# Kernel tuning notes

Hardware: AMD Instinct MI355X
Metric: run time of the kernel (lower is better)

The kernel has to match this reference:

```python
import jax, jax.numpy as jnp
import numpy as np
from jax import lax

B, L, V = 64, 48, 50000
E = 300   # emb_dim == repr_dim
F0 = 300  # fc0_dim
F1 = 300  # fc1_dim
NC = 2    # n_classes
NEG = -1e9


def setup_inputs() -> dict:
    key = jax.random.key(0)
    ks = jax.random.split(key, 16)
    inp = {
        "q1": jax.random.randint(ks[0], (B, L), 0, V, dtype=jnp.int64) if jax.config.read('jax_enable_x64') else jax.random.randint(ks[0], (B, L), 0, V, dtype=jnp.int32),
        "q2": jax.random.randint(ks[1], (B, L), 0, V, dtype=jnp.int32),
        "q1_len": jax.random.randint(ks[2], (B,), 1, L + 1, dtype=jnp.int32),
        "q2_len": jax.random.randint(ks[3], (B,), 1, L + 1, dtype=jnp.int32),
        "emb": jax.random.normal(ks[4], (V, E), jnp.float32) * 0.1,
        "conv_w": jax.random.normal(ks[5], (E, E, 3), jnp.float32) * 0.03,
        "conv_b": jnp.zeros((E,), jnp.float32),
        "fc0_w": jax.random.normal(ks[6], (F0, 2 * E), jnp.float32) * 0.04,
        "fc0_b": jnp.zeros((F0,), jnp.float32),
        "fc1_w": jax.random.normal(ks[7], (F1, 2 * F0), jnp.float32) * 0.04,
        "fc1_b": jnp.zeros((F1,), jnp.float32),
        "fc2_w": jax.random.normal(ks[8], (NC, F1), jnp.float32) * 0.05,
        "fc2_b": jnp.zeros((NC,), jnp.float32),
        "att_w": jax.random.normal(ks[9], (1, E + F0), jnp.float32) * 0.05,
        "att_b": jnp.zeros((1,), jnp.float32),
    }
    return inp


def _encode(q, emb, conv_w, conv_b):
    x = emb[q]                                   # [B, L, E]
    x = jnp.transpose(x, (0, 2, 1))              # [B, E, L] (NCW)
    y = lax.conv_general_dilated(x, conv_w, (1,), [(1, 1)],
                                 dimension_numbers=("NCW", "OIW", "NCW"))
    y = jnp.tanh(y + conv_b[None, :, None])
    return jnp.transpose(y, (0, 2, 1))           # [B, L, E]


def reference(q1, q2, q1_len, q2_len, emb, conv_w, conv_b, fc0_w, fc0_b,
              fc1_w, fc1_b, fc2_w, fc2_b, att_w, att_b):
    r1 = _encode(q1, emb, conv_w, conv_b)        # [B, L, E]
    r2 = _encode(q2, emb, conv_w, conv_b)
    pos = jnp.arange(L)
    m1 = pos[None, :] < q1_len[:, None]          # [B, L] valid-token masks
    m2 = pos[None, :] < q2_len[:, None]

    # pairwise features: |r1_i - r2_j| and r1_i * r2_j  -> fc0 -> tanh
    d = jnp.abs(r1[:, :, None, :] - r2[:, None, :, :])   # [B, L1, L2, E]
    p = r1[:, :, None, :] * r2[:, None, :, :]
    Wd, Wp = fc0_w[:, :E], fc0_w[:, E:]
    joint = jnp.tanh(jnp.einsum("bije,fe->bijf", d, Wd)
                     + jnp.einsum("bije,fe->bijf", p, Wp)
                     + fc0_b)                             # [B, L1, L2, F0]

    # masked max-pooling over the other sequence
    s1 = jnp.where(m2[:, None, :, None], joint, NEG).max(axis=2)  # [B, L1, F0]
    s2 = jnp.where(m1[:, :, None, None], joint, NEG).max(axis=1)  # [B, L2, F0]

    # attention-weighted sums (softmax over valid positions only)
    def pool(r, s, m):
        logits = jnp.einsum("bld,d->bl", jnp.concatenate([r, s], -1), att_w[0]) + att_b[0]
        a = jax.nn.softmax(jnp.where(m, logits, NEG), axis=1)     # [B, L]
        return jnp.einsum("bl,blf->bf", a, s)                     # [B, F0]

    h1 = pool(r1, s1, m1)
    h2 = pool(r2, s2, m2)

    j = jnp.tanh(jnp.concatenate([h1, h2], axis=1) @ fc1_w.T + fc1_b)
    return j @ fc2_w.T + fc2_b                                   # [B, 2]
```

## Files before the change

kernel.cpp:

```cpp
#include <hip/hip_runtime.h>
#include <math.h>

#define B_  64
#define L_  48
#define E_  300
#define F0_ 300
#define NEGP (-1e30f)
#define XROW 320
#define RS  312

typedef __attribute__((ext_vector_type(8))) _Float16 half8;
typedef __attribute__((ext_vector_type(8))) short   short8;
typedef __attribute__((ext_vector_type(4))) float   float4v;


__global__ __launch_bounds__(256) void kp_all(
    const int* __restrict__ q1, const int* __restrict__ q2,
    const float* __restrict__ emb, const float* __restrict__ conv_w,
    const float* __restrict__ fc0w,
    _Float16* __restrict__ Bp2, _Float16* __restrict__ Bc,
    _Float16* __restrict__ X)
{
    int u = blockIdx.x * 256 + threadIdx.x;
    if (u < 24320) {
        int m = u >> 8, rest = u & 255;
        int nt = rest >> 6, lane = rest & 63;
        int f = (m / 19) * 64 + nt * 16 + (lane & 15);
        int kb = (m % 19) * 32 + ((lane >> 4) << 3);
        half8 hv;
#pragma unroll
        for (int j = 0; j < 8; ++j) {
            int k = kb + j;
            float v = 0.f;
            if (f < 300) {
                if (k < 300) v = fc0w[f * 600 + k];
                else if (k >= 304 && k < 604) v = fc0w[f * 600 + k - 4];
            }
            hv[j] = (_Float16)v;
        }
        *reinterpret_cast<half8*>(Bp2 + (long)u * 8) = hv;
    } else if (u < 60800) {
        int v = u - 24320;
        int m = v / 1216, rest = v - m * 1216;
        int ntg = rest >> 6, lane = rest & 63;
        int o = ntg * 16 + (lane & 15);
        int kkb = (m % 10) * 32 + ((lane >> 4) << 3);
        int k = m / 10;
        half8 hv;
#pragma unroll
        for (int j = 0; j < 8; ++j) {
            int kk = kkb + j;
            float val = 0.f;
            if (o < 300 && kk < 300) val = conv_w[(o * 300 + kk) * 3 + k];
            hv[j] = (_Float16)val;
        }
        *reinterpret_cast<half8*>(Bc + (long)v * 8) = hv;
    } else if (u < 306560) {
        int v = u - 60800;
        int g = v / 40;
        int e8 = (v - g * 40) * 8;
        int s = g / 3072;
        int rem = g - s * 3072;
        long row = (long)((s ? q2 : q1)[rem]) * 300;
        half8 hv;
        if (e8 + 7 < 300) {
            float4 a = *reinterpret_cast<const float4*>(emb + row + e8);
            float4 c = *reinterpret_cast<const float4*>(emb + row + e8 + 4);
            hv[0] = (_Float16)a.x; hv[1] = (_Float16)a.y; hv[2] = (_Float16)a.z; hv[3] = (_Float16)a.w;
            hv[4] = (_Float16)c.x; hv[5] = (_Float16)c.y; hv[6] = (_Float16)c.z; hv[7] = (_Float16)c.w;
        } else {
#pragma unroll
            for (int j = 0; j < 8; ++j) {
                int i = e8 + j;
                hv[j] = (_Float16)((i < 300) ? emb[row + i] : 0.f);
            }
        }
        *reinterpret_cast<half8*>(X + (long)g * XROW + e8) = hv;
    }
}

__global__ __launch_bounds__(256, 4) void kc_conv(
    const _Float16* __restrict__ X, const _Float16* __restrict__ Bc,
    const float* __restrict__ conv_b, float* __restrict__ r1, float* __restrict__ r2)
{
    int wid = blockIdx.x * 4 + (threadIdx.x >> 6);
    int lane = threadIdx.x & 63;
    int mt = wid / 10;
    int pr = wid - mt * 10;
    int ntg0 = pr * 2;
    bool two = (ntg0 + 1 < 19);
    int row0 = mt * 16;
    int q = lane >> 4, jcol = lane & 15;
    int grow = row0 + jcol;
    int l = grow % 48;

    auto zero8 = []() { half8 z; for (int e = 0; e < 8; ++e) z[e] = (_Float16)0.f; return z; };
    auto loadA = [&](int m) -> half8 {
        int k = m / 10, kk0 = (m - k * 10) * 32;
        int srcl = l + k - 1;
        if (srcl >= 0 && srcl < 48)
            return *reinterpret_cast<const half8*>(X + (long)(grow + k - 1) * XROW + kk0 + q * 8);
        return zero8();
    };
    auto loadB = [&](int m, int ntg) -> half8 {
        return *reinterpret_cast<const half8*>(Bc + ((long)m * 19 + ntg) * 512 + lane * 8);
    };

    float4v acc0 = (float4v){0.f, 0.f, 0.f, 0.f};
    float4v acc1 = (float4v){0.f, 0.f, 0.f, 0.f};

    half8 a_c  = loadA(0);
    half8 b0_c = loadB(0, ntg0);
    half8 b1_c = two ? loadB(0, ntg0 + 1) : b0_c;

    for (int m = 0; m < 30; ++m) {
        half8 a_n, b0_n, b1_n;
        if (m < 29) {
            a_n  = loadA(m + 1);
            b0_n = loadB(m + 1, ntg0);
            b1_n = two ? loadB(m + 1, ntg0 + 1) : b0_n;
        } else { a_n = a_c; b0_n = b0_c; b1_n = b1_c; }
        acc0 = __builtin_amdgcn_mfma_f32_16x16x32_f16(a_c, b0_c, acc0, 0, 0, 0);
        if (two)
            acc1 = __builtin_amdgcn_mfma_f32_16x16x32_f16(a_c, b1_c, acc1, 0, 0, 0);
        a_c = a_n; b0_c = b0_n; b1_c = b1_n;
    }

#pragma unroll
    for (int t = 0; t < 2; ++t) {
        if (t == 1 && !two) break;
        int n = (ntg0 + t) * 16 + jcol;
        if (n >= 300) continue;
        float bias = conv_b[n];
        const float4v& a = t ? acc1 : acc0;
#pragma unroll
        for (int r = 0; r < 4; ++r) {
            int g = row0 + q * 4 + r;
            int s = g / 3072;
            int rem = g - s * 3072;
            float* rout = s ? r2 : r1;
            rout[(long)rem * 300 + n] = tanhf(a[r] + bias);
        }
    }
}

__global__ __launch_bounds__(256, 3) void k2_joint(
    const float* __restrict__ r1, const float* __restrict__ r2,
    const int* __restrict__ q1_len, const int* __restrict__ q2_len,
    const _Float16* __restrict__ Bp2,
    float* __restrict__ s1p, float* __restrict__ s2p)
{
    int x = blockIdx.x;
    int tile = x / 5, nc = x - tile * 5;
    int it = tile / 3, jt = tile - it * 3;
    int b = blockIdx.y;
    int tid = threadIdx.x;
    int q1l = q1_len[b], q2l = q2_len[b];
    long base1 = ((long)(b * 3 + jt) * 48 + it * 16) * 300;
    long base2 = ((long)(b * 3 + it) * 48 + jt * 16) * 300;
    bool active = (it * 16 < q1l) && (jt * 16 < q2l);
    if (!active) {
        for (int idx = tid; idx < 2048; idx += 256) {
            int side = idx >> 10;
            int rest = idx & 1023;
            int row = rest >> 6;
            int f = nc * 64 + (rest & 63);
            if (f < 300) (side ? s2p + base2 : s1p + base1)[row * 300 + f] = NEGP;
        }
        return;
    }

    __shared__ __align__(16) unsigned char smraw[16 * RS * 2 * 2];
    _Float16* r1h = (_Float16*)smraw;
    _Float16* r2h = r1h + 16 * RS;
    float* red = (float*)smraw;

    {
        const float* r1base = r1 + ((long)(b * 48) + it * 16) * 300;
        const float* r2base = r2 + ((long)(b * 48) + jt * 16) * 300;
        for (int u = tid; u < 1200; u += 256) {
            int row = u / 75;
            int e4 = (u - row * 75) * 4;
            float4 v1 = *reinterpret_cast<const float4*>(r1base + row * 300 + e4);
            float4 v2 = *reinterpret_cast<const float4*>(r2base + row * 300 + e4);
            _Float16* d1 = r1h + row * RS + e4;
            _Float16* d2 = r2h + row * RS + e4;
            d1[0] = (_Float16)v1.x; d1[1] = (_Float16)v1.y; d1[2] = (_Float16)v1.z; d1[3] = (_Float16)v1.w;
            d2[0] = (_Float16)v2.x; d2[1] = (_Float16)v2.y; d2[2] = (_Float16)v2.z; d2[3] = (_Float16)v2.w;
        }
        for (int u = tid; u < 2 * 16 * (RS - 300); u += 256) {
            int half = u / (16 * (RS - 300));
            int rest = u - half * 16 * (RS - 300);
            int row = rest / (RS - 300);
            int e = 300 + rest - row * (RS - 300);
            (half ? r2h : r1h)[row * RS + e] = (_Float16)0.f;
        }
    }
    __syncthreads();

    int w    = tid >> 6;
    int lane = tid & 63;
    int q    = lane >> 4;
    int jcol = lane & 15;

    float4v acc[4][4];
#pragma unroll
    for (int mt = 0; mt < 4; ++mt)
#pragma unroll
        for (int nt = 0; nt < 4; ++nt) acc[mt][nt] = (float4v){0.f, 0.f, 0.f, 0.f};

    const _Float16* bbase = Bp2 + (long)(nc * 19) * 2048;
    half8 b0 = *reinterpret_cast<const half8*>(bbase + lane * 8);
    half8 b1 = *reinterpret_cast<const half8*>(bbase + 512 + lane * 8);
    half8 b2 = *reinterpret_cast<const half8*>(bbase + 1024 + lane * 8);
    half8 b3 = *reinterpret_cast<const half8*>(bbase + 1536 + lane * 8);

    for (int kc = 0; kc < 19; ++kc) {
        half8 n0, n1, n2, n3;
        if (kc < 18) {
            const _Float16* nb = bbase + (long)(kc + 1) * 2048;
            n0 = *reinterpret_cast<const half8*>(nb + lane * 8);
            n1 = *reinterpret_cast<const half8*>(nb + 512 + lane * 8);
            n2 = *reinterpret_cast<const half8*>(nb + 1024 + lane * 8);
            n3 = *reinterpret_cast<const half8*>(nb + 1536 + lane * 8);
        } else { n0 = b0; n1 = b1; n2 = b2; n3 = b3; }

        int k0q = kc * 32 + q * 8;
        int koff = (k0q < 304) ? k0q : (k0q - 304);
        const half8 rv2 = *reinterpret_cast<const half8*>(r2h + jcol * RS + koff);
        half8 afr[4];
#pragma unroll
        for (int mt = 0; mt < 4; ++mt) {
            const half8 rv1 = *reinterpret_cast<const half8*>(r1h + (w * 4 + mt) * RS + koff);
            if (k0q < 304) {
                half8 dsub = rv1 - rv2;
                short8 s;
                __builtin_memcpy(&s, &dsub, 16);
                s &= (short)0x7FFF;
                __builtin_memcpy(&afr[mt], &s, 16);
            } else {
                afr[mt] = rv1 * rv2;
            }
        }
#pragma unroll
        for (int mt = 0; mt < 4; ++mt) {
            acc[mt][0] = __builtin_amdgcn_mfma_f32_16x16x32_f16(afr[mt], b0, acc[mt][0], 0, 0, 0);
            acc[mt][1] = __builtin_amdgcn_mfma_f32_16x16x32_f16(afr[mt], b1, acc[mt][1], 0, 0, 0);
            acc[mt][2] = __builtin_amdgcn_mfma_f32_16x16x32_f16(afr[mt], b2, acc[mt][2], 0, 0, 0);
            acc[mt][3] = __builtin_amdgcn_mfma_f32_16x16x32_f16(afr[mt], b3, acc[mt][3], 0, 0, 0);
        }
        b0 = n0; b1 = n1; b2 = n2; b3 = n3;
    }

#pragma unroll
    for (int mt = 0; mt < 4; ++mt) {
        int i_l = w * 4 + mt;
#pragma unroll
        for (int nt = 0; nt < 4; ++nt) {
            float mx = NEGP;
#pragma unroll
            for (int r = 0; r < 4; ++r) {
                int j = q * 4 + r;
                if (jt * 16 + j < q2l) mx = fmaxf(mx, acc[mt][nt][r]);
            }
            mx = fmaxf(mx, __shfl_xor(mx, 16));
            mx = fmaxf(mx, __shfl_xor(mx, 32));
            int f = nc * 64 + nt * 16 + jcol;
            if (q == 0 && f < 300) s1p[base1 + i_l * 300 + f] = mx;
        }
    }

    __syncthreads();
#pragma unroll
    for (int nt = 0; nt < 4; ++nt) {
#pragma unroll
        for (int r = 0; r < 4; ++r) {
            float mx = NEGP;
#pragma unroll
            for (int mt = 0; mt < 4; ++mt) {
                int i = it * 16 + w * 4 + mt;
                if (i < q1l) mx = fmaxf(mx, acc[mt][nt][r]);
            }
            red[((w * 16) + q * 4 + r) * 68 + nt * 16 + jcol] = mx;
        }
    }
    __syncthreads();
    for (int vv = tid; vv < 1024; vv += 256) {
        int j = vv >> 6;
        int fcol = vv & 63;
        float mx = red[j * 68 + fcol];
        mx = fmaxf(mx, red[(16 + j) * 68 + fcol]);
        mx = fmaxf(mx, red[(32 + j) * 68 + fcol]);
        mx = fmaxf(mx, red[(48 + j) * 68 + fcol]);
        int f = nc * 64 + fcol;
        if (f < 300) s2p[base2 + (long)j * 300 + f] = mx;
    }
}

__global__ __launch_bounds__(256) void k4_pool(
    const float* __restrict__ r1, const float* __restrict__ r2,
    const float* __restrict__ s1p, const float* __restrict__ s2p,
    const float* __restrict__ fc0b,
    const int* __restrict__ q1_len, const int* __restrict__ q2_len,
    const float* __restrict__ att_w, const float* __restrict__ att_b,
    float* __restrict__ hcat)
{
    int side = blockIdx.x >> 6;
    int b = blockIdx.x & 63;
    const float* r  = (side ? r2 : r1) + (long)b * 48 * 300;
    const float* sp = (side ? s2p : s1p) + (long)b * 43200;
    int len = (side ? q2_len : q1_len)[b];
    int tid = threadIdx.x;
    int w = tid >> 6, lane = tid & 63;
    __shared__ float sL[48 * 304];
    __shared__ float lg[48];
    __shared__ float aL[48];

    for (int u = tid; u < 14400; u += 256) {
        int l = u / 300, f = u - l * 300;
        float mx = fmaxf(fmaxf(sp[u], sp[u + 14400]), sp[u + 28800]);
        sL[l * 304 + f] = tanhf(mx + fc0b[f]);
    }
    __syncthreads();

    for (int li = 0; li < 12; ++li) {
        int l = w * 12 + li;
        float acc = 0.f;
        for (int d = lane; d < 600; d += 64) {
            float v = (d < 300) ? r[l * 300 + d] : sL[l * 304 + d - 300];
            acc += v * att_w[d];
        }
#pragma unroll
        for (int off = 32; off >= 1; off >>= 1) acc += __shfl_xor(acc, off);
        if (lane == 0) lg[l] = acc + att_b[0];
    }
    __syncthreads();

    if (tid < 64) {
        float lo = (lane < 48) ? lg[lane] : NEGP;
        float ml = (lane < len) ? lo : NEGP;
        float mx = ml;
#pragma unroll
        for (int off = 32; off >= 1; off >>= 1) mx = fmaxf(mx, __shfl_xor(mx, off));
        float ex = (lane < len) ? __expf(lo - mx) : 0.f;
        float sm = ex;
#pragma unroll
        for (int off = 32; off >= 1; off >>= 1) sm += __shfl_xor(sm, off);
        if (lane < 48) aL[lane] = ex / sm;
    }
    __syncthreads();

    for (int f = tid; f < 300; f += 256) {
        float acc = 0.f;
        for (int l = 0; l < 48; ++l) acc += aL[l] * sL[l * 304 + f];
        hcat[b * 600 + side * 300 + f] = acc;
    }
}

__global__ __launch_bounds__(256) void k5a_fc1(
    const float* __restrict__ hcat, const float* __restrict__ fc1w,
    const float* __restrict__ fc1b, float* __restrict__ jl)
{
    int wid = blockIdx.x * 4 + (threadIdx.x >> 6);
    int lane = threadIdx.x & 63;
    int b = wid / 300;
    int g = wid - b * 300;
    const float* h = hcat + (long)b * 600;
    const float* wrow = fc1w + (long)g * 600;
    float acc = 0.f;
    for (int e = lane; e < 600; e += 64)
        acc += h[e] * wrow[e];
#pragma unroll
    for (int off = 32; off >= 1; off >>= 1) acc += __shfl_xor(acc, off);
    if (lane == 0) jl[b * 300 + g] = tanhf(acc + fc1b[g]);
}

__global__ __launch_bounds__(128) void k5b_fc2(
    const float* __restrict__ jl, const float* __restrict__ fc2w,
    const float* __restrict__ fc2b, float* __restrict__ out)
{
    int b = blockIdx.x;
    int o = threadIdx.x >> 6, lane = threadIdx.x & 63;
    float acc = 0.f;
    for (int g = lane; g < 300; g += 64)
        acc += jl[b * 300 + g] * fc2w[o * 300 + g];
#pragma unroll
    for (int off = 32; off >= 1; off >>= 1) acc += __shfl_xor(acc, off);
    if (lane == 0) out[b * 2 + o] = acc + fc2b[o];
}

extern "C" void kernel_launch(void* const* d_in, const int* in_sizes, int n_in,
                              void* d_out, int out_size, void* d_ws, size_t ws_size,
                              hipStream_t stream)
{
    const int*   q1     = (const int*)d_in[0];
    const int*   q2     = (const int*)d_in[1];
    const int*   q1_len = (const int*)d_in[2];
    const int*   q2_len = (const int*)d_in[3];
    const float* emb    = (const float*)d_in[4];
    const float* conv_w = (const float*)d_in[5];
    const float* conv_b = (const float*)d_in[6];
    const float* fc0_w  = (const float*)d_in[7];
    const float* fc0_b  = (const float*)d_in[8];
    const float* fc1_w  = (const float*)d_in[9];
    const float* fc1_b  = (const float*)d_in[10];
    const float* fc2_w  = (const float*)d_in[11];
    const float* fc2_b  = (const float*)d_in[12];
    const float* att_w  = (const float*)d_in[13];
    const float* att_b  = (const float*)d_in[14];

    float* ws  = (float*)d_ws;
    float* r1  = ws;
    float* r2  = ws + 921600;
    float* s1p = ws + 1843200;
    float* s2p = ws + 4608000;
    float* hcat = ws + 9216000;
    float* jl   = ws + 9351680;
    _Float16* X   = (_Float16*)(ws + 1843200);
    _Float16* Bc  = (_Float16*)(ws + 2826240);
    _Float16* Bp2 = (_Float16*)(ws + 9254400);
    float* out = (float*)d_out;

    hipLaunchKernelGGL(kp_all, dim3(1198), dim3(256), 0, stream,
                       q1, q2, emb, conv_w, fc0_w, Bp2, Bc, X);
    hipLaunchKernelGGL(kc_conv, dim3(960), dim3(256), 0, stream,
                       X, Bc, conv_b, r1, r2);
    hipLaunchKernelGGL(k2_joint, dim3(45, 64), dim3(256), 0, stream,
                       r1, r2, q1_len, q2_len, Bp2, s1p, s2p);
    hipLaunchKernelGGL(k4_pool, dim3(128), dim3(256), 0, stream,
                       r1, r2, s1p, s2p, fc0_b, q1_len, q2_len, att_w, att_b, hcat);
    hipLaunchKernelGGL(k5a_fc1, dim3(4800), dim3(256), 0, stream,
                       hcat, fc1_w, fc1_b, jl);
    hipLaunchKernelGGL(k5b_fc2, dim3(64), dim3(128), 0, stream,
                       jl, fc2_w, fc2_b, out);
}
```

Measured before the change: 247.8 us.

## Split attention pooling into a wide combine kernel and a small softmax-pool kernel

The single 128-block pooling kernel is replaced by two kernels. The first runs one wavefront per (side, batch, position). It reduces the three partial max buffers, applies bias and tanh, writes the pooled features to global memory and computes each attention logit. The second runs 640 small blocks that each do the masked softmax over positions and a 60-column slice of the weighted sum, broadcasting the weights by shuffle. This spreads the pooling work over many more workgroups than the 128 used before, at the cost of an extra launch and a global-memory round trip for the intermediate features and logits.

```diff
diff --git a/kernel.cpp b/kernel.cpp
--- a/kernel.cpp
+++ b/kernel.cpp
@@ -297,64 +297,68 @@
     }
 }
 
-__global__ __launch_bounds__(256) void k4_pool(
+__global__ __launch_bounds__(256) void k3a_comb(
     const float* __restrict__ r1, const float* __restrict__ r2,
     const float* __restrict__ s1p, const float* __restrict__ s2p,
     const float* __restrict__ fc0b,
+    const float* __restrict__ att_w, const float* __restrict__ att_b,
+    float* __restrict__ sg1, float* __restrict__ sg2,
+    float* __restrict__ lg)
+{
+    int wid = blockIdx.x * 4 + (threadIdx.x >> 6);
+    int lane = threadIdx.x & 63;
+    int side = wid / 3072;
+    int rem = wid - side * 3072;
+    int b = rem / 48, l = rem - b * 48;
+    const float* sp = (side ? s2p : s1p) + (long)b * 43200 + l * 300;
+    const float* r  = (side ? r2 : r1) + (long)rem * 300;
+    float* sg = (side ? sg2 : sg1) + (long)rem * 300;
+
+    float lacc = 0.f;
+    for (int e = lane; e < 300; e += 64) {
+        float mx = fmaxf(fmaxf(sp[e], sp[e + 14400]), sp[e + 28800]);
+        float s = tanhf(mx + fc0b[e]);
+        sg[e] = s;
+        lacc += s * att_w[300 + e] + r[e] * att_w[e];
+    }
+#pragma unroll
+    for (int off = 32; off >= 1; off >>= 1) lacc += __shfl_xor(lacc, off);
+    if (lane == 0) lg[wid] = lacc + att_b[0];
+}
+
+__global__ __launch_bounds__(64) void k4p_pool(
+    const float* __restrict__ sg1, const float* __restrict__ sg2,
+    const float* __restrict__ lg,
     const int* __restrict__ q1_len, const int* __restrict__ q2_len,
-    const float* __restrict__ att_w, const float* __restrict__ att_b,
     float* __restrict__ hcat)
 {
-    int side = blockIdx.x >> 6;
-    int b = blockIdx.x & 63;
-    const float* r  = (side ? r2 : r1) + (long)b * 48 * 300;
-    const float* sp = (side ? s2p : s1p) + (long)b * 43200;
+    int bid = blockIdx.x;
+    int side = bid / 320;
+    int rest = bid - side * 320;
+    int b = rest / 5, fc = rest - b * 5;
+    int lane = threadIdx.x;
     int len = (side ? q2_len : q1_len)[b];
-    int tid = threadIdx.x;
-    int w = tid >> 6, lane = tid & 63;
-    __shared__ float sL[48 * 304];
-    __shared__ float lg[48];
-    __shared__ float aL[48];
-
-    for (int u = tid; u < 14400; u += 256) {
-        int l = u / 300, f = u - l * 300;
-        float mx = fmaxf(fmaxf(sp[u], sp[u + 14400]), sp[u + 28800]);
-        sL[l * 304 + f] = tanhf(mx + fc0b[f]);
-    }
-    __syncthreads();
-
-    for (int li = 0; li < 12; ++li) {
-        int l = w * 12 + li;
-        float acc = 0.f;
-        for (int d = lane; d < 600; d += 64) {
-            float v = (d < 300) ? r[l * 300 + d] : sL[l * 304 + d - 300];
-            acc += v * att_w[d];
-        }
-#pragma unroll
-        for (int off = 32; off >= 1; off >>= 1) acc += __shfl_xor(acc, off);
-        if (lane == 0) lg[l] = acc + att_b[0];
-    }
-    __syncthreads();
-
-    if (tid < 64) {
-        float lo = (lane < 48) ? lg[lane] : NEGP;
-        float ml = (lane < len) ? lo : NEGP;
-        float mx = ml;
-#pragma unroll
-        for (int off = 32; off >= 1; off >>= 1) mx = fmaxf(mx, __shfl_xor(mx, off));
-        float ex = (lane < len) ? __expf(lo - mx) : 0.f;
-        float sm = ex;
-#pragma unroll
-        for (int off = 32; off >= 1; off >>= 1) sm += __shfl_xor(sm, off);
-        if (lane < 48) aL[lane] = ex / sm;
-    }
-    __syncthreads();
-
-    for (int f = tid; f < 300; f += 256) {
-        float acc = 0.f;
-        for (int l = 0; l < 48; ++l) acc += aL[l] * sL[l * 304 + f];
+    const float* sg = (side ? sg2 : sg1) + (long)b * 48 * 300;
+
+    float lo = (lane < 48) ? lg[(side * 64 + b) * 48 + lane] : NEGP;
+    float ml = (lane < len) ? lo : NEGP;
+    float mx = ml;
+#pragma unroll
+    for (int off = 32; off >= 1; off >>= 1) mx = fmaxf(mx, __shfl_xor(mx, off));
+    float ex = (lane < len) ? __expf(lo - mx) : 0.f;
+    float sm = ex;
+#pragma unroll
+    for (int off = 32; off >= 1; off >>= 1) sm += __shfl_xor(sm, off);
+    float aLv = ex / sm;
+
+    int f = fc * 60 + lane;
+    float acc = 0.f;
+    for (int l = 0; l < 48; ++l) {
+        float a = __shfl(aLv, l);
+        if (f < 300) acc += a * sg[(long)l * 300 + f];
+    }
+    if (f < 300 && lane < 60)
         hcat[b * 600 + side * 300 + f] = acc;
-    }
 }
 
 __global__ __launch_bounds__(256) void k5a_fc1(
@@ -414,8 +418,11 @@
     float* r2  = ws + 921600;
     float* s1p = ws + 1843200;
     float* s2p = ws + 4608000;
+    float* sg1 = ws + 7372800;
+    float* sg2 = ws + 8294400;
     float* hcat = ws + 9216000;
     float* jl   = ws + 9351680;
+    float* lg   = ws + 9370880;
     _Float16* X   = (_Float16*)(ws + 1843200);
     _Float16* Bc  = (_Float16*)(ws + 2826240);
     _Float16* Bp2 = (_Float16*)(ws + 9254400);
@@ -427,8 +434,10 @@
                        X, Bc, conv_b, r1, r2);
     hipLaunchKernelGGL(k2_joint, dim3(45, 64), dim3(256), 0, stream,
                        r1, r2, q1_len, q2_len, Bp2, s1p, s2p);
-    hipLaunchKernelGGL(k4_pool, dim3(128), dim3(256), 0, stream,
-                       r1, r2, s1p, s2p, fc0_b, q1_len, q2_len, att_w, att_b, hcat);
+    hipLaunchKernelGGL(k3a_comb, dim3(1536), dim3(256), 0, stream,
+                       r1, r2, s1p, s2p, fc0_b, att_w, att_b, sg1, sg2, lg);
+    hipLaunchKernelGGL(k4p_pool, dim3(640), dim3(64), 0, stream,
+                       sg1, sg2, lg, q1_len, q2_len, hcat);
     hipLaunchKernelGGL(k5a_fc1, dim3(4800), dim3(256), 0, stream,
                        hcat, fc1_w, fc1_b, jl);
     hipLaunchKernelGGL(k5b_fc2, dim3(64), dim3(128), 0, stream,
```

Result: faster. 217.9 us (-12.0%).
